# Performance work log

Measured on AMD Instinct MI355X. Metric: run time of the kernel, lower is better.

## Reference

```python
import jax, jax.numpy as jnp
import numpy as np

N, D, C = 4096, 512, 100
EPS = 1e-8


def setup_inputs() -> dict:
    key = jax.random.key(0)
    k1, k2 = jax.random.split(key)
    X = jax.random.normal(k1, (N, D), dtype=jnp.float32)
    # torch.rand -> uniform [0, 1), shape (1, hiddensize, classes)
    grp = jax.random.uniform(k2, (1, D, C), dtype=jnp.float32)
    return {"X": X, "grp": grp}


def reference(X, grp):
    # L1 distance of each sample to each class prototype: [N, D, 1] - [1, D, C] -> sum over D -> [N, C]
    l1 = jnp.abs(X[:, :, None] - grp).sum(axis=1)
    norm = jax.nn.softmax(-l1, axis=1)  # Softmin over classes

    # Cosine similarity between X [N, D] and prototypes grp[0] [D, C] -> [N, C]
    g = grp[0]
    dot = X @ g  # [N, C]
    xn = jnp.sqrt(jnp.sum(X * X, axis=1, keepdims=True))      # [N, 1]
    gn = jnp.sqrt(jnp.sum(g * g, axis=0, keepdims=True))      # [1, C]
    cs = dot / jnp.maximum(xn * gn, EPS)

    confidence = jnp.max(cs, axis=1, keepdims=True)  # [N, 1]
    confusion = jax.nn.softmax(cs, axis=1)           # [N, C]
    return confidence * confusion * norm
```

## Files before the change

### kernel.cpp

```cpp
#include <hip/hip_runtime.h>

#define D_DIM 512
#define C_CLS 100
#define SAMP 4
#define NT 256

__global__ __launch_bounds__(128) void gn_kernel(const float* __restrict__ grp,
                                                 float* __restrict__ gn) {
    __shared__ float4 red[128];
    const int t = threadIdx.x;
    const int cb = blockIdx.x * 4;
    float4 acc = {0.f, 0.f, 0.f, 0.f};
    for (int d = t; d < D_DIM; d += 128) {
        float4 g = *(const float4*)&grp[d * C_CLS + cb];
        acc.x = fmaf(g.x, g.x, acc.x);
        acc.y = fmaf(g.y, g.y, acc.y);
        acc.z = fmaf(g.z, g.z, acc.z);
        acc.w = fmaf(g.w, g.w, acc.w);
    }
    red[t] = acc;
    __syncthreads();
    for (int off = 64; off > 0; off >>= 1) {
        if (t < off) {
            float4 a = red[t], b = red[t + off];
            a.x += b.x; a.y += b.y; a.z += b.z; a.w += b.w;
            red[t] = a;
        }
        __syncthreads();
    }
    if (t == 0) {
        float4 a = red[0];
        gn[cb + 0] = sqrtf(a.x);
        gn[cb + 1] = sqrtf(a.y);
        gn[cb + 2] = sqrtf(a.z);
        gn[cb + 3] = sqrtf(a.w);
    }
}

__global__ __launch_bounds__(NT, 4) void cls_kernel(const float* __restrict__ X,
                                                    const float* __restrict__ grp,
                                                    const float* __restrict__ gn,
                                                    float* __restrict__ out) {
    __shared__ float xs[SAMP][520];
    __shared__ float part[8][25][36];
    __shared__ float redA[SAMP][25];
    __shared__ float redB[SAMP][25];
    __shared__ float xsqs[SAMP];

    const int t = threadIdx.x;
    const int n0 = blockIdx.x * SAMP;

    {
        const float4* Xv = (const float4*)(X + (size_t)n0 * D_DIM);
#pragma unroll
        for (int i = t; i < SAMP * D_DIM / 4; i += NT) {
            int row = i >> 7;
            int col = i & 127;
            *(float4*)&xs[row][col * 4] = Xv[i];
        }
    }
    __syncthreads();

    if (t < 128) {
        const int r = t >> 5, j = t & 31;
        float v = 0.f;
#pragma unroll
        for (int k = 0; k < 4; ++k) {
            float4 a = *(const float4*)&xs[r][j * 4 + k * 128];
            v += a.x * a.x + a.y * a.y + a.z * a.z + a.w * a.w;
        }
#pragma unroll
        for (int m = 16; m > 0; m >>= 1) v += __shfl_xor(v, m, 32);
        if (j == 0) xsqs[r] = v;
    }

    const bool act = (t < 200);
    const int dq = t / 25;
    const int cq = t - dq * 25;

    float l1[4][4];
    float dt[4][4];
#pragma unroll
    for (int i = 0; i < 4; ++i)
#pragma unroll
        for (int j = 0; j < 4; ++j) { l1[i][j] = 0.f; dt[i][j] = 0.f; }

    if (act) {
        const float* gp = grp + cq * 4;
        const int dbase = dq * 64;
#pragma unroll 4
        for (int dd = 0; dd < 64; dd += 4) {
            const int d4 = dbase + dd;
            float xr[4][4];
#pragma unroll
            for (int si = 0; si < 4; ++si)
                *(float4*)&xr[si][0] = *(const float4*)&xs[si][d4];
#pragma unroll
            for (int k = 0; k < 4; ++k) {
                float4 g = *(const float4*)&gp[(d4 + k) * C_CLS];
                float ga[4] = {g.x, g.y, g.z, g.w};
#pragma unroll
                for (int si = 0; si < 4; ++si) {
                    float x = xr[si][k];
#pragma unroll
                    for (int c = 0; c < 4; ++c) {
                        l1[si][c] += fabsf(x - ga[c]);
                        dt[si][c] = fmaf(x, ga[c], dt[si][c]);
                    }
                }
            }
        }
        float* p = &part[dq][cq][0];
#pragma unroll
        for (int si = 0; si < 4; ++si) {
            *(float4*)&p[si * 4]      = *(float4*)&l1[si][0];
            *(float4*)&p[16 + si * 4] = *(float4*)&dt[si][0];
        }
    }
    __syncthreads();

    const int s  = t / 25;
    const int c2 = t - s * 25;
    const bool act2 = (t < 100);

    float l1c[4] = {0.f, 0.f, 0.f, 0.f};
    float dtc[4] = {0.f, 0.f, 0.f, 0.f};
    if (act2) {
#pragma unroll
        for (int q = 0; q < 8; ++q) {
            const float* p = &part[q][c2][0];
            float4 a = *(const float4*)&p[s * 4];
            float4 b = *(const float4*)&p[16 + s * 4];
            l1c[0] += a.x; l1c[1] += a.y; l1c[2] += a.z; l1c[3] += a.w;
            dtc[0] += b.x; dtc[1] += b.y; dtc[2] += b.z; dtc[3] += b.w;
        }
    }

    float cs[4] = {0.f, 0.f, 0.f, 0.f};
    if (act2) {
        float xn = sqrtf(xsqs[s]);
        float4 gv = *(const float4*)&gn[c2 * 4];
        cs[0] = dtc[0] / fmaxf(xn * gv.x, 1e-8f);
        cs[1] = dtc[1] / fmaxf(xn * gv.y, 1e-8f);
        cs[2] = dtc[2] / fmaxf(xn * gv.z, 1e-8f);
        cs[3] = dtc[3] / fmaxf(xn * gv.w, 1e-8f);
        redA[s][c2] = fminf(fminf(l1c[0], l1c[1]), fminf(l1c[2], l1c[3]));
        redB[s][c2] = fmaxf(fmaxf(cs[0], cs[1]), fmaxf(cs[2], cs[3]));
    }
    __syncthreads();

    float minl1 = 0.f, maxcs = 0.f;
    if (act2) {
        minl1 = redA[s][0];
        maxcs = redB[s][0];
        for (int k = 1; k < 25; ++k) {
            minl1 = fminf(minl1, redA[s][k]);
            maxcs = fmaxf(maxcs, redB[s][k]);
        }
    }
    __syncthreads();

    if (act2) {
        redA[s][c2] = __expf(minl1 - l1c[0]) + __expf(minl1 - l1c[1]) +
                      __expf(minl1 - l1c[2]) + __expf(minl1 - l1c[3]);
        redB[s][c2] = __expf(cs[0] - maxcs) + __expf(cs[1] - maxcs) +
                      __expf(cs[2] - maxcs) + __expf(cs[3] - maxcs);
    }
    __syncthreads();

    if (act2) {
        float s1 = 0.f, s2 = 0.f;
        for (int k = 0; k < 25; ++k) { s1 += redA[s][k]; s2 += redB[s][k]; }
        float f = maxcs / (s1 * s2);
        float4 o;
        o.x = f * __expf(cs[0] - maxcs) * __expf(minl1 - l1c[0]);
        o.y = f * __expf(cs[1] - maxcs) * __expf(minl1 - l1c[1]);
        o.z = f * __expf(cs[2] - maxcs) * __expf(minl1 - l1c[2]);
        o.w = f * __expf(cs[3] - maxcs) * __expf(minl1 - l1c[3]);
        *(float4*)&out[(size_t)(n0 + s) * C_CLS + c2 * 4] = o;
    }
}

extern "C" void kernel_launch(void* const* d_in, const int* in_sizes, int n_in,
                              void* d_out, int out_size, void* d_ws, size_t ws_size,
                              hipStream_t stream) {
    const float* X   = (const float*)d_in[0];
    const float* grp = (const float*)d_in[1];
    float* out = (float*)d_out;
    float* gn  = (float*)d_ws;

    gn_kernel<<<25, 128, 0, stream>>>(grp, gn);
    cls_kernel<<<4096 / SAMP, NT, 0, stream>>>(X, grp, gn, out);
}
```

Measured before the change: 35.91 us.

## Fuse prototype-norm computation into main kernel and use packed float2 math

```diff
diff --git a/kernel.cpp b/kernel.cpp
--- a/kernel.cpp
+++ b/kernel.cpp
@@ -1,45 +1,14 @@
 #include <hip/hip_runtime.h>
+
+typedef float v2f __attribute__((ext_vector_type(2)));
 
 #define D_DIM 512
 #define C_CLS 100
 #define SAMP 4
 #define NT 256
 
-__global__ __launch_bounds__(128) void gn_kernel(const float* __restrict__ grp,
-                                                 float* __restrict__ gn) {
-    __shared__ float4 red[128];
-    const int t = threadIdx.x;
-    const int cb = blockIdx.x * 4;
-    float4 acc = {0.f, 0.f, 0.f, 0.f};
-    for (int d = t; d < D_DIM; d += 128) {
-        float4 g = *(const float4*)&grp[d * C_CLS + cb];
-        acc.x = fmaf(g.x, g.x, acc.x);
-        acc.y = fmaf(g.y, g.y, acc.y);
-        acc.z = fmaf(g.z, g.z, acc.z);
-        acc.w = fmaf(g.w, g.w, acc.w);
-    }
-    red[t] = acc;
-    __syncthreads();
-    for (int off = 64; off > 0; off >>= 1) {
-        if (t < off) {
-            float4 a = red[t], b = red[t + off];
-            a.x += b.x; a.y += b.y; a.z += b.z; a.w += b.w;
-            red[t] = a;
-        }
-        __syncthreads();
-    }
-    if (t == 0) {
-        float4 a = red[0];
-        gn[cb + 0] = sqrtf(a.x);
-        gn[cb + 1] = sqrtf(a.y);
-        gn[cb + 2] = sqrtf(a.z);
-        gn[cb + 3] = sqrtf(a.w);
-    }
-}
-
 __global__ __launch_bounds__(NT, 4) void cls_kernel(const float* __restrict__ X,
                                                     const float* __restrict__ grp,
-                                                    const float* __restrict__ gn,
                                                     float* __restrict__ out) {
     __shared__ float xs[SAMP][520];
     __shared__ float part[8][25][36];
@@ -79,16 +48,20 @@
     const int cq = t - dq * 25;
 
     float l1[4][4];
-    float dt[4][4];
+    v2f dtl[4], dth[4];
+    v2f gsql = {0.f, 0.f}, gsqh = {0.f, 0.f};
 #pragma unroll
-    for (int i = 0; i < 4; ++i)
+    for (int i = 0; i < 4; ++i) {
+        dtl[i] = (v2f){0.f, 0.f};
+        dth[i] = (v2f){0.f, 0.f};
 #pragma unroll
-        for (int j = 0; j < 4; ++j) { l1[i][j] = 0.f; dt[i][j] = 0.f; }
+        for (int j = 0; j < 4; ++j) l1[i][j] = 0.f;
+    }
 
     if (act) {
         const float* gp = grp + cq * 4;
         const int dbase = dq * 64;
-#pragma unroll 4
+#pragma unroll 2
         for (int dd = 0; dd < 64; dd += 4) {
             const int d4 = dbase + dd;
             float xr[4][4];
@@ -98,24 +71,32 @@
 #pragma unroll
             for (int k = 0; k < 4; ++k) {
                 float4 g = *(const float4*)&gp[(d4 + k) * C_CLS];
-                float ga[4] = {g.x, g.y, g.z, g.w};
+                v2f glo = {g.x, g.y};
+                v2f ghi = {g.z, g.w};
+                gsql += glo * glo;
+                gsqh += ghi * ghi;
 #pragma unroll
                 for (int si = 0; si < 4; ++si) {
                     float x = xr[si][k];
-#pragma unroll
-                    for (int c = 0; c < 4; ++c) {
-                        l1[si][c] += fabsf(x - ga[c]);
-                        dt[si][c] = fmaf(x, ga[c], dt[si][c]);
-                    }
+                    v2f x2 = {x, x};
+                    v2f el = x2 - glo;
+                    v2f eh = x2 - ghi;
+                    l1[si][0] += fabsf(el.x);
+                    l1[si][1] += fabsf(el.y);
+                    l1[si][2] += fabsf(eh.x);
+                    l1[si][3] += fabsf(eh.y);
+                    dtl[si] += x2 * glo;
+                    dth[si] += x2 * ghi;
                 }
             }
         }
         float* p = &part[dq][cq][0];
 #pragma unroll
         for (int si = 0; si < 4; ++si) {
-            *(float4*)&p[si * 4]      = *(float4*)&l1[si][0];
-            *(float4*)&p[16 + si * 4] = *(float4*)&dt[si][0];
+            *(float4*)&p[si * 4]      = float4{l1[si][0], l1[si][1], l1[si][2], l1[si][3]};
+            *(float4*)&p[16 + si * 4] = float4{dtl[si].x, dtl[si].y, dth[si].x, dth[si].y};
         }
+        *(float4*)&p[32] = float4{gsql.x, gsql.y, gsqh.x, gsqh.y};
     }
     __syncthreads();
 
@@ -125,25 +106,26 @@
 
     float l1c[4] = {0.f, 0.f, 0.f, 0.f};
     float dtc[4] = {0.f, 0.f, 0.f, 0.f};
+    float gsc[4] = {0.f, 0.f, 0.f, 0.f};
     if (act2) {
 #pragma unroll
         for (int q = 0; q < 8; ++q) {
             const float* p = &part[q][c2][0];
             float4 a = *(const float4*)&p[s * 4];
             float4 b = *(const float4*)&p[16 + s * 4];
+            float4 c = *(const float4*)&p[32];
             l1c[0] += a.x; l1c[1] += a.y; l1c[2] += a.z; l1c[3] += a.w;
             dtc[0] += b.x; dtc[1] += b.y; dtc[2] += b.z; dtc[3] += b.w;
+            gsc[0] += c.x; gsc[1] += c.y; gsc[2] += c.z; gsc[3] += c.w;
         }
     }
 
     float cs[4] = {0.f, 0.f, 0.f, 0.f};
     if (act2) {
-        float xn = sqrtf(xsqs[s]);
-        float4 gv = *(const float4*)&gn[c2 * 4];
-        cs[0] = dtc[0] / fmaxf(xn * gv.x, 1e-8f);
-        cs[1] = dtc[1] / fmaxf(xn * gv.y, 1e-8f);
-        cs[2] = dtc[2] / fmaxf(xn * gv.z, 1e-8f);
-        cs[3] = dtc[3] / fmaxf(xn * gv.w, 1e-8f);
+        float xq = xsqs[s];
+#pragma unroll
+        for (int c = 0; c < 4; ++c)
+            cs[c] = dtc[c] / fmaxf(sqrtf(xq * gsc[c]), 1e-8f);
         redA[s][c2] = fminf(fminf(l1c[0], l1c[1]), fminf(l1c[2], l1c[3]));
         redB[s][c2] = fmaxf(fmaxf(cs[0], cs[1]), fmaxf(cs[2], cs[3]));
     }
@@ -187,8 +169,7 @@
     const float* X   = (const float*)d_in[0];
     const float* grp = (const float*)d_in[1];
     float* out = (float*)d_out;
-    float* gn  = (float*)d_ws;
+    (void)d_ws; (void)ws_size;
 
-    gn_kernel<<<25, 128, 0, stream>>>(grp, gn);
-    cls_kernel<<<4096 / SAMP, NT, 0, stream>>>(X, grp, gn, out);
+    cls_kernel<<<4096 / SAMP, NT, 0, stream>>>(X, grp, out);
 }
```

Result: faster. 32.90 us (-8.4%).
